# Kernel tuning notes

Measured on AMD Instinct MI355X. Metric: run time of the kernel, lower is better.

Reference implementation:

```python
import jax, jax.numpy as jnp
import numpy as np

NUM_FEATURES = 64
SCALE = 10.0


def setup_inputs() -> dict:
    key = jax.random.key(0)
    k1, k2, k3, k4 = jax.random.split(key, 4)
    fractions = jax.random.uniform(k1, (4, 1024), dtype=jnp.float32)
    W = jax.random.normal(k2, (1, NUM_FEATURES), dtype=jnp.float32) * 0.1
    b = jax.random.uniform(k3, (NUM_FEATURES,), dtype=jnp.float32) * (2.0 * np.pi)
    a = jax.random.normal(k4, (NUM_FEATURES,), dtype=jnp.float32)
    return {"fractions": fractions, "W": W, "b": b, "a": a}


def reference(fractions, W, b, a):
    # diffs: [B, N, N]
    diffs = fractions[:, None, :] - fractions[:, :, None]
    scaled = diffs * SCALE
    # rff: [B, N, N, F] = cos(scaled[..., None] * W[0] + b)
    rff = jnp.cos(scaled[..., None] * W[0] + b)
    # weighted reduction over features -> [B, N, N]
    positional_bias = jnp.einsum("bijf,f->bij", rff, a)
    return positional_bias
```

## Files before the change

kernel.cpp:

```cpp
#include <hip/hip_runtime.h>
#include <hip/hip_bf16.h>

#define NPOS   1024
#define NBATCH 4
#define RT     128
#define LDT    136
#define CLD    68

typedef _Float16 half8  __attribute__((ext_vector_type(8)));
typedef _Float16 half2x __attribute__((ext_vector_type(2)));
typedef float    floatx4 __attribute__((ext_vector_type(4)));

#define INV2PI 0.15915494309189535f

__global__ __launch_bounds__(256, 1)
void fourier_bias_kernel(const float* __restrict__ frac,
                         const float* __restrict__ Wv,
                         const float* __restrict__ bv,
                         const float* __restrict__ av,
                         float* __restrict__ out) {
    __shared__ _Float16 sA[RT][LDT];
    __shared__ _Float16 sB[RT][LDT];
    __shared__ float    sC[4][16][CLD];
    __shared__ float    sXA[RT], sXB[RT];

    const int tid = threadIdx.x;
    const int bz  = blockIdx.z;
    const int ti  = blockIdx.y * RT;
    const int tj  = blockIdx.x * RT;

    const float* fb = frac + bz * NPOS;
    if (tid < 128) sXA[tid]       = fb[ti + tid];
    else           sXB[tid - 128] = fb[tj + (tid - 128)];

    const int   f      = tid & 63;
    const int   rt4    = tid >> 6;
    const float wf_rev = Wv[f] * (10.0f * INV2PI);
    const float bf_rev = bv[f] * INV2PI;
    const float af     = av[f];
    __syncthreads();

    #pragma unroll
    for (int t = 0; t < 32; ++t) {
        const int row = rt4 + t * 4;
        const float ai = sXA[row] * wf_rev;
        half2x pa;
        pa[0] = (_Float16)__builtin_amdgcn_cosf(ai);
        pa[1] = (_Float16)__builtin_amdgcn_sinf(ai);
        *reinterpret_cast<half2x*>(&sA[row][2 * f]) = pa;
        const float aj = __builtin_fmaf(sXB[row], wf_rev, bf_rev);
        half2x pb;
        pb[0] = (_Float16)(af * __builtin_amdgcn_cosf(aj));
        pb[1] = (_Float16)(af * __builtin_amdgcn_sinf(aj));
        *reinterpret_cast<half2x*>(&sB[row][2 * f]) = pb;
    }
    __syncthreads();

    const int lane = tid & 63;
    const int wid  = tid >> 6;
    const int wr   = (wid >> 1) * 64;
    const int wc   = (wid & 1) * 64;
    const int lrow = lane & 15;
    const int lkb  = lane >> 4;
    const int rhi  = (lane >> 4) * 4;

    half8 bfr[4][4];
    #pragma unroll
    for (int t = 0; t < 4; ++t)
        #pragma unroll
        for (int n = 0; n < 4; ++n)
            bfr[t][n] = *reinterpret_cast<const half8*>(
                &sB[wc + n * 16 + lrow][t * 32 + lkb * 8]);

    #pragma unroll
    for (int m = 0; m < 4; ++m) {
        floatx4 acc[4];
        #pragma unroll
        for (int n = 0; n < 4; ++n) acc[n] = (floatx4){0.f, 0.f, 0.f, 0.f};

        #pragma unroll
        for (int t = 0; t < 4; ++t) {
            const half8 afr = *reinterpret_cast<const half8*>(
                &sA[wr + m * 16 + lrow][t * 32 + lkb * 8]);
            #pragma unroll
            for (int n = 0; n < 4; ++n)
                acc[n] = __builtin_amdgcn_mfma_f32_16x16x32_f16(
                    afr, bfr[t][n], acc[n], 0, 0, 0);
        }

        #pragma unroll
        for (int n = 0; n < 4; ++n)
            #pragma unroll
            for (int r = 0; r < 4; ++r)
                sC[wid][rhi + r][n * 16 + lrow] = acc[n][r];

        #pragma unroll
        for (int q = 0; q < 4; ++q) {
            const int row16 = q * 4 + (lane >> 4);
            const int c4    = lrow * 4;
            const floatx4 v = *reinterpret_cast<const floatx4*>(&sC[wid][row16][c4]);
            const size_t gi = (size_t)(ti + wr + m * 16 + row16);
            const size_t gj = (size_t)(tj + wc + c4);
            __builtin_nontemporal_store(
                v, reinterpret_cast<floatx4*>(out + ((size_t)bz * NPOS + gi) * NPOS + gj));
        }
    }
}

extern "C" void kernel_launch(void* const* d_in, const int* in_sizes, int n_in,
                              void* d_out, int out_size, void* d_ws, size_t ws_size,
                              hipStream_t stream) {
    const float* frac = (const float*)d_in[0];
    const float* Wv   = (const float*)d_in[1];
    const float* bv   = (const float*)d_in[2];
    const float* av   = (const float*)d_in[3];
    float* out = (float*)d_out;

    dim3 grid(NPOS / RT, NPOS / RT, NBATCH);
    fourier_bias_kernel<<<grid, dim3(256), 0, stream>>>(frac, Wv, bv, av, out);
}
```

Measured before the change: 11.22 us.

## Split trig precompute and GEMM into two kernels via workspace

Computes each position's cos/sin feature rows once into a swizzled fp16 workspace, then runs a separate GEMM kernel with 64x64 tiles. That kernel loads the tiles with global_load_lds, uses an XOR-swizzled LDS layout and remaps workgroup order. Both it and the fallback fused kernel drop the LDS-staged nontemporal vector stores in favour of direct scalar stores. This removes the trig work that the old kernel repeated in every tile and raises occupancy, at the cost of a second launch, a workspace round trip and less coalesced output writes.

After: 16.14 us. 43.9% more time.

```diff
diff --git a/kernel.cpp b/kernel.cpp
--- a/kernel.cpp
+++ b/kernel.cpp
@@ -3,9 +3,9 @@
 
 #define NPOS   1024
 #define NBATCH 4
-#define RT     128
-#define LDT    136
-#define CLD    68
+#define BT     64
+#define KD     128
+#define ROWB   256
 
 typedef _Float16 half8  __attribute__((ext_vector_type(8)));
 typedef _Float16 half2x __attribute__((ext_vector_type(2)));
@@ -13,33 +13,135 @@
 
 #define INV2PI 0.15915494309189535f
 
+
+__device__ __forceinline__ void gload_lds16(const void* g, void* l) {
+    __builtin_amdgcn_global_load_lds(
+        (const __attribute__((address_space(1))) void*)g,
+        (__attribute__((address_space(3))) void*)l, 16, 0, 0);
+}
+
+__global__ __launch_bounds__(256)
+void trig_kernel(const float* __restrict__ frac, const float* __restrict__ Wv,
+                 const float* __restrict__ bv,   const float* __restrict__ av,
+                 _Float16* __restrict__ wsA, _Float16* __restrict__ wsB) {
+    const int g = blockIdx.x * 256 + threadIdx.x;
+    const int f = g & 63;
+    const int p = (g >> 6) & (NPOS - 1);
+    const int b = g >> 16;
+    const float x  = frac[(b << 10) + p];
+    const float wf = Wv[f] * (10.0f * INV2PI);
+    const float bf = bv[f] * INV2PI;
+    const float af = av[f];
+
+    const unsigned rowbase = (unsigned)(((b << 10) + p) * ROWB);
+    const unsigned off     = ((unsigned)(f * 4)) ^ (((unsigned)(p & 7)) << 4);
+
+    const float ai = x * wf;
+    half2x pa;
+    pa[0] = (_Float16)__builtin_amdgcn_cosf(ai);
+    pa[1] = (_Float16)__builtin_amdgcn_sinf(ai);
+    *reinterpret_cast<half2x*>(reinterpret_cast<char*>(wsA) + rowbase + off) = pa;
+
+    const float aj = __builtin_fmaf(x, wf, bf);
+    half2x pb;
+    pb[0] = (_Float16)(af * __builtin_amdgcn_cosf(aj));
+    pb[1] = (_Float16)(af * __builtin_amdgcn_sinf(aj));
+    *reinterpret_cast<half2x*>(reinterpret_cast<char*>(wsB) + rowbase + off) = pb;
+}
+
+__global__ __launch_bounds__(256, 4)
+void gemm_kernel(const _Float16* __restrict__ wsA, const _Float16* __restrict__ wsB,
+                 float* __restrict__ out) {
+    __shared__ _Float16 sA[BT * KD];
+    __shared__ _Float16 sB[BT * KD];
+
+    int wg = blockIdx.x;
+    wg = (wg & 7) * 128 + (wg >> 3);
+    const int bz  = wg >> 8;
+    const int rem = wg & 255;
+    const int ti  = (rem >> 4) * BT;
+    const int tj  = (rem & 15) * BT;
+
+    const int tid  = threadIdx.x;
+    const int lane = tid & 63;
+    const int wid  = tid >> 6;
+
+    const char* gA = reinterpret_cast<const char*>(wsA) + (size_t)((bz << 10) + ti) * ROWB;
+    const char* gB = reinterpret_cast<const char*>(wsB) + (size_t)((bz << 10) + tj) * ROWB;
+    #pragma unroll
+    for (int q = 0; q < 4; ++q) {
+        const int c = wid * 4 + q;
+        gload_lds16(gA + c * 1024 + lane * 16, reinterpret_cast<char*>(sA) + c * 1024);
+        gload_lds16(gB + c * 1024 + lane * 16, reinterpret_cast<char*>(sB) + c * 1024);
+    }
+    __syncthreads();
+
+    const int wr   = (wid >> 1) * 32;
+    const int wc   = (wid & 1) * 32;
+    const int lrow = lane & 15;
+    const int lkb  = lane >> 4;
+
+    half8 afr[2][4], bfr[2][4];
+    #pragma unroll
+    for (int m = 0; m < 2; ++m)
+        #pragma unroll
+        for (int t = 0; t < 4; ++t) {
+            const int ra = wr + m * 16 + lrow;
+            const unsigned Ga = (unsigned)(t * 64 + lkb * 16) ^ (((unsigned)(ra & 7)) << 4);
+            afr[m][t] = *reinterpret_cast<const half8*>(
+                reinterpret_cast<const char*>(sA) + ra * ROWB + Ga);
+            const int rb = wc + m * 16 + lrow;
+            const unsigned Gb = (unsigned)(t * 64 + lkb * 16) ^ (((unsigned)(rb & 7)) << 4);
+            bfr[m][t] = *reinterpret_cast<const half8*>(
+                reinterpret_cast<const char*>(sB) + rb * ROWB + Gb);
+        }
+
+    const int rhi = (lane >> 4) * 4;
+    #pragma unroll
+    for (int m = 0; m < 2; ++m) {
+        floatx4 acc[2];
+        #pragma unroll
+        for (int n = 0; n < 2; ++n) acc[n] = (floatx4){0.f, 0.f, 0.f, 0.f};
+        #pragma unroll
+        for (int t = 0; t < 4; ++t)
+            #pragma unroll
+            for (int n = 0; n < 2; ++n)
+                acc[n] = __builtin_amdgcn_mfma_f32_16x16x32_f16(
+                    afr[m][t], bfr[n][t], acc[n], 0, 0, 0);
+        #pragma unroll
+        for (int n = 0; n < 2; ++n) {
+            const size_t gj = (size_t)(tj + wc + n * 16 + lrow);
+            #pragma unroll
+            for (int r = 0; r < 4; ++r) {
+                const size_t gi = (size_t)(ti + wr + m * 16 + rhi + r);
+                out[((size_t)bz * NPOS + gi) * NPOS + gj] = acc[n][r];
+            }
+        }
+    }
+}
+
+#define RT  128
+#define LDT 136
 __global__ __launch_bounds__(256, 1)
-void fourier_bias_kernel(const float* __restrict__ frac,
-                         const float* __restrict__ Wv,
-                         const float* __restrict__ bv,
-                         const float* __restrict__ av,
-                         float* __restrict__ out) {
+void fused_kernel(const float* __restrict__ frac, const float* __restrict__ Wv,
+                  const float* __restrict__ bv,   const float* __restrict__ av,
+                  float* __restrict__ out) {
     __shared__ _Float16 sA[RT][LDT];
     __shared__ _Float16 sB[RT][LDT];
-    __shared__ float    sC[4][16][CLD];
     __shared__ float    sXA[RT], sXB[RT];
-
     const int tid = threadIdx.x;
     const int bz  = blockIdx.z;
     const int ti  = blockIdx.y * RT;
     const int tj  = blockIdx.x * RT;
-
     const float* fb = frac + bz * NPOS;
-    if (tid < 128) sXA[tid]       = fb[ti + tid];
+    if (tid < 128) sXA[tid] = fb[ti + tid];
     else           sXB[tid - 128] = fb[tj + (tid - 128)];
-
     const int   f      = tid & 63;
     const int   rt4    = tid >> 6;
     const float wf_rev = Wv[f] * (10.0f * INV2PI);
     const float bf_rev = bv[f] * INV2PI;
     const float af     = av[f];
     __syncthreads();
-
     #pragma unroll
     for (int t = 0; t < 32; ++t) {
         const int row = rt4 + t * 4;
@@ -55,15 +157,9 @@
         *reinterpret_cast<half2x*>(&sB[row][2 * f]) = pb;
     }
     __syncthreads();
-
-    const int lane = tid & 63;
-    const int wid  = tid >> 6;
-    const int wr   = (wid >> 1) * 64;
-    const int wc   = (wid & 1) * 64;
-    const int lrow = lane & 15;
-    const int lkb  = lane >> 4;
-    const int rhi  = (lane >> 4) * 4;
-
+    const int lane = tid & 63, wid = tid >> 6;
+    const int wr = (wid >> 1) * 64, wc = (wid & 1) * 64;
+    const int lrow = lane & 15, lkb = lane >> 4, rhi = (lane >> 4) * 4;
     half8 bfr[4][4];
     #pragma unroll
     for (int t = 0; t < 4; ++t)
@@ -71,13 +167,11 @@
         for (int n = 0; n < 4; ++n)
             bfr[t][n] = *reinterpret_cast<const half8*>(
                 &sB[wc + n * 16 + lrow][t * 32 + lkb * 8]);
-
     #pragma unroll
     for (int m = 0; m < 4; ++m) {
         floatx4 acc[4];
         #pragma unroll
         for (int n = 0; n < 4; ++n) acc[n] = (floatx4){0.f, 0.f, 0.f, 0.f};
-
         #pragma unroll
         for (int t = 0; t < 4; ++t) {
             const half8 afr = *reinterpret_cast<const half8*>(
@@ -87,22 +181,14 @@
                 acc[n] = __builtin_amdgcn_mfma_f32_16x16x32_f16(
                     afr, bfr[t][n], acc[n], 0, 0, 0);
         }
-
-        #pragma unroll
-        for (int n = 0; n < 4; ++n)
-            #pragma unroll
-            for (int r = 0; r < 4; ++r)
-                sC[wid][rhi + r][n * 16 + lrow] = acc[n][r];
-
-        #pragma unroll
-        for (int q = 0; q < 4; ++q) {
-            const int row16 = q * 4 + (lane >> 4);
-            const int c4    = lrow * 4;
-            const floatx4 v = *reinterpret_cast<const floatx4*>(&sC[wid][row16][c4]);
-            const size_t gi = (size_t)(ti + wr + m * 16 + row16);
-            const size_t gj = (size_t)(tj + wc + c4);
-            __builtin_nontemporal_store(
-                v, reinterpret_cast<floatx4*>(out + ((size_t)bz * NPOS + gi) * NPOS + gj));
+        #pragma unroll
+        for (int n = 0; n < 4; ++n) {
+            const size_t gj = (size_t)(tj + wc + n * 16 + lrow);
+            #pragma unroll
+            for (int r = 0; r < 4; ++r) {
+                const size_t gi = (size_t)(ti + wr + m * 16 + rhi + r);
+                out[((size_t)bz * NPOS + gi) * NPOS + gj] = acc[n][r];
+            }
         }
     }
 }
@@ -116,6 +202,14 @@
     const float* av   = (const float*)d_in[3];
     float* out = (float*)d_out;
 
-    dim3 grid(NPOS / RT, NPOS / RT, NBATCH);
-    fourier_bias_kernel<<<grid, dim3(256), 0, stream>>>(frac, Wv, bv, av, out);
-}
+    const size_t need = (size_t)NBATCH * NPOS * ROWB * 2;
+    if (ws_size >= need) {
+        _Float16* wsA = (_Float16*)d_ws;
+        _Float16* wsB = (_Float16*)((char*)d_ws + need / 2);
+        trig_kernel<<<dim3(1024), dim3(256), 0, stream>>>(frac, Wv, bv, av, wsA, wsB);
+        gemm_kernel<<<dim3(1024), dim3(256), 0, stream>>>(wsA, wsB, out);
+    } else {
+        dim3 grid(NPOS / RT, NPOS / RT, NBATCH);
+        fused_kernel<<<grid, dim3(256), 0, stream>>>(frac, Wv, bv, av, out);
+    }
+}
```
